# Performance work log

Hardware: AMD Instinct MI355X
Metric: run time of the kernel (lower is better)

## Reference

```python
import jax, jax.numpy as jnp
import numpy as np

B, IN_DIM, HID, OUT = 4096, 2048, 2048, 2048
BN_EPS = 1e-5


def setup_inputs() -> dict:
    key = jax.random.key(0)
    ks = jax.random.split(key, 4)
    s1 = 1.0 / np.sqrt(IN_DIM)
    s2 = 1.0 / np.sqrt(HID)
    return {
        "x1": jax.random.normal(ks[0], (B, IN_DIM), jnp.float32),
        "x2": jax.random.normal(ks[1], (B, IN_DIM), jnp.float32),
        "W1": jax.random.normal(ks[2], (IN_DIM, HID), jnp.float32) * s1,
        "b1": jnp.zeros((HID,), jnp.float32),
        "gamma": jnp.ones((HID,), jnp.float32),
        "beta": jnp.zeros((HID,), jnp.float32),
        "W2": jax.random.normal(ks[3], (HID, OUT), jnp.float32) * s2,
        "b2": jnp.zeros((OUT,), jnp.float32),
        "batch_size": B,
        "T": jnp.float32(0.2),
    }


def _predictor(x, W1, b1, gamma, beta, W2, b2):
    # Linear -> BatchNorm1d (training-mode batch stats, biased var) -> ReLU -> Linear
    h = x @ W1 + b1
    mu = jnp.mean(h, axis=0)
    var = jnp.var(h, axis=0)  # biased, matches torch BN normalization
    h = (h - mu) * jax.lax.rsqrt(var + BN_EPS) * gamma + beta
    h = jax.nn.relu(h)
    return h @ W2 + b2


def _off_diag(S):
    # S: [B, B] -> [B, B-1], row i keeps columns j != i (order preserved)
    n = S.shape[0]
    j = jnp.arange(n - 1)
    cols = j[None, :] + (j[None, :] >= jnp.arange(n)[:, None])
    return jnp.take_along_axis(S, cols, axis=1)


def _l2norm(x):
    return x / jnp.linalg.norm(x, axis=1, keepdims=True)


def reference(x1, x2, W1, b1, gamma, beta, W2, b2, batch_size, T):
    q1 = _l2norm(_predictor(x1, W1, b1, gamma, beta, W2, b2))
    q2 = _l2norm(_predictor(x2, W1, b1, gamma, beta, W2, b2))
    k1, k2 = q1, q2  # k = normalized q in the original

    l_pos1 = jnp.sum(q1 * k2, axis=1)  # [B]
    l_pos2 = jnp.sum(q2 * k1, axis=1)

    # per-row negatives: cat(q without self, k_other without self)
    neg1 = jnp.concatenate([_off_diag(q1 @ q1.T), _off_diag(q1 @ k2.T)], axis=1)
    neg2 = jnp.concatenate([_off_diag(q2 @ q2.T), _off_diag(q2 @ k1.T)], axis=1)

    logits1 = jnp.concatenate([l_pos1[:, None], neg1], axis=1) / T  # [B, 2B-1]
    logits2 = jnp.concatenate([l_pos2[:, None], neg2], axis=1) / T
    labels = jnp.zeros((q1.shape[0],), jnp.int32)
    return logits1, logits2, labels
```

## Files before the change

### kernel.cpp

```cpp
#include <hip/hip_runtime.h>
#include <stdint.h>

#define BATCH 4096
#define DIM   2048
#define LROW  8191

typedef __attribute__((ext_vector_type(8))) short bf16x8;
typedef __attribute__((ext_vector_type(4))) float f32x4;

typedef __attribute__((address_space(1))) void gvoid;
typedef __attribute__((address_space(3))) void lvoid;
#define GLOAD16(g, l) __builtin_amdgcn_global_load_lds((gvoid*)(g), (lvoid*)(l), 16, 0, 0)

__device__ __forceinline__ unsigned short f2bf(float f) {
    unsigned int u = __float_as_uint(f);
    return (unsigned short)((u + 0x7FFFu + ((u >> 16) & 1u)) >> 16);
}
__device__ __forceinline__ float bf2f(unsigned short s) {
    return __uint_as_float(((unsigned int)s) << 16);
}


__global__ __launch_bounds__(256) void k_cvt8(const float* __restrict__ src,
                                              unsigned short* __restrict__ dst) {
    size_t i = ((size_t)blockIdx.x * 256 + threadIdx.x) * 8;
    float4 v0 = *(const float4*)(src + i);
    float4 v1 = *(const float4*)(src + i + 4);
    bf16x8 p;
    p[0] = (short)f2bf(v0.x); p[1] = (short)f2bf(v0.y);
    p[2] = (short)f2bf(v0.z); p[3] = (short)f2bf(v0.w);
    p[4] = (short)f2bf(v1.x); p[5] = (short)f2bf(v1.y);
    p[6] = (short)f2bf(v1.z); p[7] = (short)f2bf(v1.w);
    *(bf16x8*)(dst + i) = p;
}

__global__ __launch_bounds__(256) void k_transpose_cvt(const float* __restrict__ W,
                                                       unsigned short* __restrict__ WT) {
    __shared__ unsigned short t[32][33];
    int n0 = blockIdx.x * 32, k0 = blockIdx.y * 32;
    int tx = threadIdx.x, ty = threadIdx.y;
#pragma unroll
    for (int i = 0; i < 4; i++) {
        int k = ty + i * 8;
        t[k][tx] = f2bf(W[(size_t)(k0 + k) * DIM + n0 + tx]);
    }
    __syncthreads();
#pragma unroll
    for (int i = 0; i < 4; i++) {
        int r = ty + i * 8;
        WT[(size_t)(n0 + r) * DIM + k0 + tx] = t[tx][r];
    }
}

template <int EPI>
__global__ __launch_bounds__(256) void k_gemm(const short* __restrict__ A_,
                                              const short* __restrict__ B_,
                                              void* __restrict__ out0,
                                              void* __restrict__ out1,
                                              const float* __restrict__ bias,
                                              float* __restrict__ st0,
                                              float* __restrict__ st1,
                                              const float* __restrict__ Tptr,
                                              int K) {
    __shared__ __align__(16) short smem[2 * 128 * 32];
    short* As = smem;
    short* Bs = smem + 128 * 32;

    const int tid = threadIdx.x;
    const int w = tid >> 6, l = tid & 63;
    const int wRow = (w >> 1) * 64, wCol = (w & 1) * 64;
    const int lr = l & 15, quad = l >> 4;

    int m0, n0, bi = 0, bj = 0;
    const short* A;
    const short* Bm;
    if (EPI == 2) {
        int t = blockIdx.x;
        while (t >= 32 - bi) { t -= 32 - bi; bi++; }
        bj = bi + t;
        m0 = bi * 128; n0 = bj * 128;
        const short* Q = A_ + (size_t)blockIdx.y * BATCH * DIM;
        A = Q; Bm = Q;
    } else {
        m0 = blockIdx.y * 128; n0 = blockIdx.x * 128;
        A = A_; Bm = B_;
    }

    const int c0 = w * 2, c1 = w * 2 + 1;
    const int lrow = l >> 2, lkoff = (l & 3) * 8;
    const short* gA0 = A + (size_t)(m0 + c0 * 16 + lrow) * K + lkoff;
    const short* gA1 = A + (size_t)(m0 + c1 * 16 + lrow) * K + lkoff;
    const short* gB0 = Bm + (size_t)(n0 + c0 * 16 + lrow) * K + lkoff;
    const short* gB1 = Bm + (size_t)(n0 + c1 * 16 + lrow) * K + lkoff;
    short* lA0 = As + c0 * 512; short* lA1 = As + c1 * 512;
    short* lB0 = Bs + c0 * 512; short* lB1 = Bs + c1 * 512;

    const int aoff = (wRow + lr) * 32 + quad * 8;
    const int boff = (wCol + lr) * 32 + quad * 8;

    f32x4 acc[4][4] = {};

    for (int k0 = 0; k0 < K; k0 += 32) {
        GLOAD16(gA0, lA0); GLOAD16(gA1, lA1);
        GLOAD16(gB0, lB0); GLOAD16(gB1, lB1);
        gA0 += 32; gA1 += 32; gB0 += 32; gB1 += 32;
        __syncthreads();

        bf16x8 af[4], bfr[4];
#pragma unroll
        for (int i = 0; i < 4; i++) {
            af[i]  = *(const bf16x8*)(As + aoff + i * 512);
            bfr[i] = *(const bf16x8*)(Bs + boff + i * 512);
        }
#pragma unroll
        for (int mi = 0; mi < 4; mi++)
#pragma unroll
            for (int ni = 0; ni < 4; ni++)
                acc[mi][ni] = __builtin_amdgcn_mfma_f32_16x16x32_bf16(af[mi], bfr[ni],
                                                                      acc[mi][ni], 0, 0, 0);
        __syncthreads();
    }

    if (EPI == 0) {
        unsigned short* H = (unsigned short*)out0;
        const int half = m0 >> 12;
        float s[4] = {0.f, 0.f, 0.f, 0.f}, s2[4] = {0.f, 0.f, 0.f, 0.f};
#pragma unroll
        for (int ni = 0; ni < 4; ni++) {
            int col = n0 + wCol + ni * 16 + lr;
            float bv = bias[col];
#pragma unroll
            for (int mi = 0; mi < 4; mi++) {
                int row = m0 + wRow + mi * 16 + quad * 4;
#pragma unroll
                for (int r = 0; r < 4; r++) {
                    float v = acc[mi][ni][r] + bv;
                    H[(size_t)(row + r) * DIM + col] = f2bf(v);
                    s[ni] += v; s2[ni] += v * v;
                }
            }
        }
#pragma unroll
        for (int ni = 0; ni < 4; ni++) {
            float a = s[ni], b = s2[ni];
            a += __shfl_xor(a, 16); b += __shfl_xor(b, 16);
            a += __shfl_xor(a, 32); b += __shfl_xor(b, 32);
            if (quad == 0) {
                int col = n0 + wCol + ni * 16 + lr;
                atomicAdd(&st0[half * DIM + col], a);
                atomicAdd(&st1[half * DIM + col], b);
            }
        }
    } else if (EPI == 1) {
        unsigned short* G = (unsigned short*)out0;
        float bv[4];
#pragma unroll
        for (int ni = 0; ni < 4; ni++) bv[ni] = bias[n0 + wCol + ni * 16 + lr];
#pragma unroll
        for (int mi = 0; mi < 4; mi++) {
            int rowb = m0 + wRow + mi * 16 + quad * 4;
#pragma unroll
            for (int r = 0; r < 4; r++) {
                int row = rowb + r;
                float p = 0.f;
#pragma unroll
                for (int ni = 0; ni < 4; ni++) {
                    int col = n0 + wCol + ni * 16 + lr;
                    float v = acc[mi][ni][r] + bv[ni];
                    G[(size_t)row * DIM + col] = f2bf(v);
                    p += v * v;
                }
                p += __shfl_xor(p, 1); p += __shfl_xor(p, 2);
                p += __shfl_xor(p, 4); p += __shfl_xor(p, 8);
                if (lr == 0) atomicAdd(&st0[row], p);
            }
        }
    } else {
        const float invT = 1.0f / Tptr[0];
        float* L  = (EPI == 2) ? (float*)(blockIdx.y ? out1 : out0) : (float*)out0;
        float* Lm = (EPI == 2) ? L : (float*)out1;
        const bool diagblk = (EPI == 2) && (bi == bj);
#pragma unroll
        for (int mi = 0; mi < 4; mi++) {
            int ibase = m0 + wRow + mi * 16 + quad * 4;
#pragma unroll
            for (int ni = 0; ni < 4; ni++) {
                int j = n0 + wCol + ni * 16 + lr;
#pragma unroll
                for (int r = 0; r < 4; r++) {
                    int i = ibase + r;
                    float v = acc[mi][ni][r] * invT;
                    int dc;
                    if (EPI == 2) {
                        if (diagblk) {
                            if (j == i) continue;
                            dc = 1 + j - (j > i);
                        } else {
                            dc = j;
                        }
                    } else {
                        dc = (j == i) ? 0 : (4096 + j - (j > i));
                    }
                    L[(size_t)i * LROW + dc] = v;
                }
            }
        }
        if (EPI == 3 || bi != bj) {
            float* tsc = (float*)smem + w * 320;
#pragma unroll
            for (int mi = 0; mi < 4; mi++) {
                int I0 = m0 + wRow + mi * 16;
#pragma unroll
                for (int ni = 0; ni < 4; ni++) {
                    int J0 = n0 + wCol + ni * 16;
#pragma unroll
                    for (int r = 0; r < 4; r++)
                        tsc[(quad * 4 + r) * 20 + lr] = acc[mi][ni][r];
                    int a = I0 + lr;
#pragma unroll
                    for (int r = 0; r < 4; r++) {
                        int b = J0 + quad * 4 + r;
                        float tv = tsc[lr * 20 + quad * 4 + r] * invT;
                        int dcm;
                        if (EPI == 2) dcm = 1 + a;
                        else dcm = (a == b) ? 0 : (4096 + a - (a > b));
                        Lm[(size_t)b * LROW + dcm] = tv;
                    }
                }
            }
        }
    }
}


__global__ __launch_bounds__(256) void k_bn_coef(float* __restrict__ musum,
                                                 float* __restrict__ sqsum,
                                                 const float* __restrict__ gamma,
                                                 const float* __restrict__ beta) {
    int i = blockIdx.x * 256 + threadIdx.x;
    int col = i & (DIM - 1);
    const float inv_n = 1.0f / 4096.0f;
    float mu = musum[i] * inv_n;
    float var = sqsum[i] * inv_n - mu * mu;
    float sc = rsqrtf(var + 1e-5f) * gamma[col];
    musum[i] = sc;
    sqsum[i] = beta[col] - mu * sc;
}

__global__ __launch_bounds__(256) void k_bn_apply(unsigned short* __restrict__ H,
                                                  const float* __restrict__ scale,
                                                  const float* __restrict__ shift) {
    size_t idx = ((size_t)blockIdx.x * 256 + threadIdx.x) * 8;
    int col = (int)(idx & (DIM - 1));
    int base = ((int)(idx >> 23)) * DIM + col;
    bf16x8 hv = *(bf16x8*)(H + idx);
    bf16x8 o;
#pragma unroll
    for (int t = 0; t < 8; t++) {
        float x = bf2f((unsigned short)hv[t]);
        x = fmaxf(x * scale[base + t] + shift[base + t], 0.f);
        o[t] = (short)f2bf(x);
    }
    *(bf16x8*)(H + idx) = o;
}

__global__ __launch_bounds__(256) void k_rowinv(float* __restrict__ rss) {
    int i = blockIdx.x * 256 + threadIdx.x;
    rss[i] = rsqrtf(rss[i]);
}

__global__ __launch_bounds__(256) void k_qnorm(const unsigned short* __restrict__ G,
                                               const float* __restrict__ inv,
                                               unsigned short* __restrict__ Q) {
    size_t idx = ((size_t)blockIdx.x * 256 + threadIdx.x) * 8;
    float iv = inv[idx >> 11];
    bf16x8 g = *(const bf16x8*)(G + idx);
    bf16x8 o;
#pragma unroll
    for (int t = 0; t < 8; t++) o[t] = (short)f2bf(bf2f((unsigned short)g[t]) * iv);
    *(bf16x8*)(Q + idx) = o;
}


extern "C" void kernel_launch(void* const* d_in, const int* in_sizes, int n_in,
                              void* d_out, int out_size, void* d_ws, size_t ws_size,
                              hipStream_t stream) {
    const float* x1    = (const float*)d_in[0];
    const float* x2    = (const float*)d_in[1];
    const float* W1    = (const float*)d_in[2];
    const float* b1    = (const float*)d_in[3];
    const float* gamma = (const float*)d_in[4];
    const float* beta  = (const float*)d_in[5];
    const float* W2    = (const float*)d_in[6];
    const float* b2    = (const float*)d_in[7];
    const float* Tp    = (const float*)d_in[9];
    float* out = (float*)d_out;

    char* ws = (char*)d_ws;
    unsigned short* R1  = (unsigned short*)ws;
    unsigned short* R3  = (unsigned short*)(ws + (32ull << 20));
    unsigned short* W1T = (unsigned short*)(ws + (64ull << 20));
    unsigned short* W2T = (unsigned short*)(ws + (72ull << 20));
    float* musum = (float*)(ws + (80ull << 20));
    float* sqsum = musum + 2 * DIM;
    float* rss   = sqsum + 2 * DIM;

    hipMemsetAsync(musum, 0, (4 * DIM + 8192) * sizeof(float), stream);

    k_cvt8<<<4096, 256, 0, stream>>>(x1, R1);
    k_cvt8<<<4096, 256, 0, stream>>>(x2, R1 + (size_t)BATCH * DIM);
    k_transpose_cvt<<<dim3(64, 64), dim3(32, 8), 0, stream>>>(W1, W1T);
    k_transpose_cvt<<<dim3(64, 64), dim3(32, 8), 0, stream>>>(W2, W2T);

    k_gemm<0><<<dim3(16, 64), 256, 0, stream>>>((const short*)R1, (const short*)W1T,
                                                R3, nullptr, b1, musum, sqsum, nullptr, DIM);
    k_bn_coef<<<16, 256, 0, stream>>>(musum, sqsum, gamma, beta);
    k_bn_apply<<<8192, 256, 0, stream>>>(R3, musum, sqsum);

    k_gemm<1><<<dim3(16, 64), 256, 0, stream>>>((const short*)R3, (const short*)W2T,
                                                R1, nullptr, b2, rss, nullptr, nullptr, DIM);
    k_rowinv<<<32, 256, 0, stream>>>(rss);
    k_qnorm<<<8192, 256, 0, stream>>>(R1, rss, R3);

    const short* Q  = (const short*)R3;
    const short* Q2 = (const short*)(R3 + (size_t)BATCH * DIM);
    float* L1 = out;
    float* L2 = out + (size_t)BATCH * LROW;
    k_gemm<2><<<dim3(528, 2), 256, 0, stream>>>(Q, nullptr, L1, L2,
                                                nullptr, nullptr, nullptr, Tp, DIM);
    k_gemm<3><<<dim3(32, 32), 256, 0, stream>>>(Q, Q2, L1, L2,
                                                nullptr, nullptr, nullptr, Tp, DIM);

    hipMemsetAsync(out + (size_t)2 * BATCH * LROW, 0, BATCH * sizeof(int), stream);
}
```

Measured before the change: 831.6 us.

## Use 256x256 tiled pipelined GEMM, fold L2 normalization into logits epilogue

Replaces the 128x128 GEMM with a 512-thread 256x256 tile kernel that uses a multi-stage LDS ring of global-to-LDS loads, XOR-swizzled LDS addressing, and MFMA priority hints. The separate q-normalization pass is removed: the similarity GEMM now runs on unnormalized rows and scales each output by the inverse row norms in the epilogue. All four similarity blocks (q1q1, q1q2, q2q1, q2q2) become one symmetric upper-triangular launch over the stacked 8192 rows, with mirrored writes. This aims for more data reuse per tile and fewer kernel launches and passes, at the cost of 128 KB of LDS, higher register pressure, and a slightly different rounding order.

```diff
diff --git a/kernel.cpp b/kernel.cpp
--- a/kernel.cpp
+++ b/kernel.cpp
@@ -53,87 +53,140 @@
 }
 
 template <int EPI>
-__global__ __launch_bounds__(256) void k_gemm(const short* __restrict__ A_,
-                                              const short* __restrict__ B_,
-                                              void* __restrict__ out0,
-                                              void* __restrict__ out1,
-                                              const float* __restrict__ bias,
-                                              float* __restrict__ st0,
-                                              float* __restrict__ st1,
-                                              const float* __restrict__ Tptr,
-                                              int K) {
-    __shared__ __align__(16) short smem[2 * 128 * 32];
-    short* As = smem;
-    short* Bs = smem + 128 * 32;
-
-    const int tid = threadIdx.x;
-    const int w = tid >> 6, l = tid & 63;
-    const int wRow = (w >> 1) * 64, wCol = (w & 1) * 64;
-    const int lr = l & 15, quad = l >> 4;
+__global__ __launch_bounds__(512, 2) void k_g256(const short* __restrict__ A_,
+                                                 const short* __restrict__ B_,
+                                                 void* __restrict__ out0,
+                                                 void* __restrict__ out1,
+                                                 const float* __restrict__ bias,
+                                                 float* __restrict__ st0,
+                                                 float* __restrict__ st1,
+                                                 const float* __restrict__ Tptr,
+                                                 int K) {
+    __shared__ __align__(16) char smem[131072];
+
+    const int tid  = threadIdx.x;
+    const int w    = tid >> 6;
+    const int l    = tid & 63;
+    const int lr   = l & 15;
+    const int quad = l >> 4;
+    const int wm   = w >> 2;
+    const int wn   = w & 3;
 
     int m0, n0, bi = 0, bj = 0;
-    const short* A;
-    const short* Bm;
     if (EPI == 2) {
         int t = blockIdx.x;
         while (t >= 32 - bi) { t -= 32 - bi; bi++; }
         bj = bi + t;
-        m0 = bi * 128; n0 = bj * 128;
-        const short* Q = A_ + (size_t)blockIdx.y * BATCH * DIM;
-        A = Q; Bm = Q;
+        m0 = bi * 256; n0 = bj * 256;
     } else {
-        m0 = blockIdx.y * 128; n0 = blockIdx.x * 128;
-        A = A_; Bm = B_;
-    }
-
-    const int c0 = w * 2, c1 = w * 2 + 1;
-    const int lrow = l >> 2, lkoff = (l & 3) * 8;
-    const short* gA0 = A + (size_t)(m0 + c0 * 16 + lrow) * K + lkoff;
-    const short* gA1 = A + (size_t)(m0 + c1 * 16 + lrow) * K + lkoff;
-    const short* gB0 = Bm + (size_t)(n0 + c0 * 16 + lrow) * K + lkoff;
-    const short* gB1 = Bm + (size_t)(n0 + c1 * 16 + lrow) * K + lkoff;
-    short* lA0 = As + c0 * 512; short* lA1 = As + c1 * 512;
-    short* lB0 = Bs + c0 * 512; short* lB1 = Bs + c1 * 512;
-
-    const int aoff = (wRow + lr) * 32 + quad * 8;
-    const int boff = (wCol + lr) * 32 + quad * 8;
-
-    f32x4 acc[4][4] = {};
-
-    for (int k0 = 0; k0 < K; k0 += 32) {
-        GLOAD16(gA0, lA0); GLOAD16(gA1, lA1);
-        GLOAD16(gB0, lB0); GLOAD16(gB1, lB1);
-        gA0 += 32; gA1 += 32; gB0 += 32; gB1 += 32;
-        __syncthreads();
-
-        bf16x8 af[4], bfr[4];
-#pragma unroll
-        for (int i = 0; i < 4; i++) {
-            af[i]  = *(const bf16x8*)(As + aoff + i * 512);
-            bfr[i] = *(const bf16x8*)(Bs + boff + i * 512);
-        }
-#pragma unroll
-        for (int mi = 0; mi < 4; mi++)
-#pragma unroll
-            for (int ni = 0; ni < 4; ni++)
-                acc[mi][ni] = __builtin_amdgcn_mfma_f32_16x16x32_bf16(af[mi], bfr[ni],
-                                                                      acc[mi][ni], 0, 0, 0);
-        __syncthreads();
-    }
+        m0 = blockIdx.y * 256; n0 = blockIdx.x * 256;
+    }
+
+    const int NT = K >> 6;
+    const size_t rsb = (size_t)K * 2;
+
+    const unsigned soff = (unsigned)((w * 1024 + l * 16) ^ (l & 32));
+    const int rowS = soff >> 6;
+    const int kbS  = soff & 63;
+    const char* APan = (const char*)A_ + (size_t)(m0 + rowS) * rsb + kbS;
+    const char* BPan = (const char*)B_ + (size_t)(n0 + rowS) * rsb + kbS;
+    const size_t row128 = rsb << 7;
+    char* ldsS = smem + w * 1024;
+
+    const int laneoff = (lr * 64 + quad * 16) ^ ((lr & 8) << 2);
+    const char* ldsA = smem + wm * 8192 + laneoff;
+    const char* ldsB = smem + wn * 4096 + laneoff;
+
+    f32x4 acc[8][4] = {};
+    bf16x8 aq[4], bq[4];
+
+    auto STAGE = [&](int ht) {
+        if (ht < 4 * NT) {
+            const size_t koff = (size_t)((ht >> 2) * 128 + ((ht >> 1) & 1) * 64);
+            char* d = ldsS + ((ht & 7) << 14);
+            const char* s = (ht & 1) ? (APan + koff) : (BPan + koff);
+            GLOAD16(s, d);
+            GLOAD16(s + row128, d + 8192);
+        }
+    };
+
+#define MM16(mh)                                                                     \
+    _Pragma("unroll") for (int mi = 0; mi < 4; ++mi) {                               \
+        _Pragma("unroll") for (int ni = 0; ni < 4; ++ni) {                           \
+            acc[(mh) * 4 + mi][ni] = __builtin_amdgcn_mfma_f32_16x16x32_bf16(        \
+                aq[mi], bq[ni], acc[(mh) * 4 + mi][ni], 0, 0, 0);                    \
+        }                                                                            \
+    }
+#define BAR()   __builtin_amdgcn_s_barrier()
+#define LGKM0() asm volatile("s_waitcnt lgkmcnt(0)" ::: "memory")
+
+    for (int ht = 0; ht < 7; ++ht) STAGE(ht);
+    asm volatile("s_waitcnt vmcnt(6)" ::: "memory");
+    BAR();
+
+    int htn = 7;
+    for (int t = 0; t < NT; ++t) {
+        const int s0 = (t & 1) << 2;
+#pragma unroll
+        for (int ni = 0; ni < 4; ++ni)
+            bq[ni] = *(const bf16x8*)(ldsB + (s0 << 14) + ni * 1024);
+#pragma unroll
+        for (int mi = 0; mi < 4; ++mi)
+            aq[mi] = *(const bf16x8*)(ldsA + ((s0 + 1) << 14) + mi * 1024);
+        STAGE(htn); ++htn;
+        BAR(); LGKM0();
+        __builtin_amdgcn_s_setprio(1);
+        MM16(0)
+        __builtin_amdgcn_s_setprio(0);
+        BAR();
+#pragma unroll
+        for (int mi = 0; mi < 4; ++mi)
+            aq[mi] = *(const bf16x8*)(ldsA + ((s0 + 1) << 14) + 4096 + mi * 1024);
+        STAGE(htn); ++htn;
+        BAR(); LGKM0();
+        __builtin_amdgcn_s_setprio(1);
+        MM16(1)
+        __builtin_amdgcn_s_setprio(0);
+        BAR();
+#pragma unroll
+        for (int ni = 0; ni < 4; ++ni)
+            bq[ni] = *(const bf16x8*)(ldsB + ((s0 + 2) << 14) + ni * 1024);
+#pragma unroll
+        for (int mi = 0; mi < 4; ++mi)
+            aq[mi] = *(const bf16x8*)(ldsA + ((s0 + 3) << 14) + mi * 1024);
+        STAGE(htn); ++htn;
+        BAR(); LGKM0();
+        __builtin_amdgcn_s_setprio(1);
+        MM16(0)
+        __builtin_amdgcn_s_setprio(0);
+        BAR();
+#pragma unroll
+        for (int mi = 0; mi < 4; ++mi)
+            aq[mi] = *(const bf16x8*)(ldsA + ((s0 + 3) << 14) + 4096 + mi * 1024);
+        STAGE(htn); ++htn;
+        BAR(); LGKM0();
+        __builtin_amdgcn_s_setprio(1);
+        MM16(1)
+        __builtin_amdgcn_s_setprio(0);
+        if (t < NT - 2) { asm volatile("s_waitcnt vmcnt(6)" ::: "memory"); }
+        else            { asm volatile("s_waitcnt vmcnt(0)" ::: "memory"); }
+        BAR();
+    }
+#undef MM16
 
     if (EPI == 0) {
         unsigned short* H = (unsigned short*)out0;
         const int half = m0 >> 12;
-        float s[4] = {0.f, 0.f, 0.f, 0.f}, s2[4] = {0.f, 0.f, 0.f, 0.f};
-#pragma unroll
-        for (int ni = 0; ni < 4; ni++) {
-            int col = n0 + wCol + ni * 16 + lr;
-            float bv = bias[col];
-#pragma unroll
-            for (int mi = 0; mi < 4; mi++) {
-                int row = m0 + wRow + mi * 16 + quad * 4;
-#pragma unroll
-                for (int r = 0; r < 4; r++) {
+        float s[4] = {}, s2[4] = {};
+#pragma unroll
+        for (int ni = 0; ni < 4; ++ni) {
+            const int col = n0 + wn * 64 + ni * 16 + lr;
+            const float bv = bias[col];
+#pragma unroll
+            for (int mi = 0; mi < 8; ++mi) {
+                const int row = m0 + wm * 128 + mi * 16 + quad * 4;
+#pragma unroll
+                for (int r = 0; r < 4; ++r) {
                     float v = acc[mi][ni][r] + bv;
                     H[(size_t)(row + r) * DIM + col] = f2bf(v);
                     s[ni] += v; s2[ni] += v * v;
@@ -141,12 +194,12 @@
             }
         }
 #pragma unroll
-        for (int ni = 0; ni < 4; ni++) {
+        for (int ni = 0; ni < 4; ++ni) {
             float a = s[ni], b = s2[ni];
             a += __shfl_xor(a, 16); b += __shfl_xor(b, 16);
             a += __shfl_xor(a, 32); b += __shfl_xor(b, 32);
             if (quad == 0) {
-                int col = n0 + wCol + ni * 16 + lr;
+                const int col = n0 + wn * 64 + ni * 16 + lr;
                 atomicAdd(&st0[half * DIM + col], a);
                 atomicAdd(&st1[half * DIM + col], b);
             }
@@ -155,17 +208,17 @@
         unsigned short* G = (unsigned short*)out0;
         float bv[4];
 #pragma unroll
-        for (int ni = 0; ni < 4; ni++) bv[ni] = bias[n0 + wCol + ni * 16 + lr];
-#pragma unroll
-        for (int mi = 0; mi < 4; mi++) {
-            int rowb = m0 + wRow + mi * 16 + quad * 4;
-#pragma unroll
-            for (int r = 0; r < 4; r++) {
-                int row = rowb + r;
+        for (int ni = 0; ni < 4; ++ni) bv[ni] = bias[n0 + wn * 64 + ni * 16 + lr];
+#pragma unroll
+        for (int mi = 0; mi < 8; ++mi) {
+            const int rowb = m0 + wm * 128 + mi * 16 + quad * 4;
+#pragma unroll
+            for (int r = 0; r < 4; ++r) {
+                const int row = rowb + r;
                 float p = 0.f;
 #pragma unroll
-                for (int ni = 0; ni < 4; ni++) {
-                    int col = n0 + wCol + ni * 16 + lr;
+                for (int ni = 0; ni < 4; ++ni) {
+                    const int col = n0 + wn * 64 + ni * 16 + lr;
                     float v = acc[mi][ni][r] + bv[ni];
                     G[(size_t)row * DIM + col] = f2bf(v);
                     p += v * v;
@@ -177,59 +230,72 @@
         }
     } else {
         const float invT = 1.0f / Tptr[0];
-        float* L  = (EPI == 2) ? (float*)(blockIdx.y ? out1 : out0) : (float*)out0;
-        float* Lm = (EPI == 2) ? L : (float*)out1;
-        const bool diagblk = (EPI == 2) && (bi == bj);
-#pragma unroll
-        for (int mi = 0; mi < 4; mi++) {
-            int ibase = m0 + wRow + mi * 16 + quad * 4;
-#pragma unroll
-            for (int ni = 0; ni < 4; ni++) {
-                int j = n0 + wCol + ni * 16 + lr;
-#pragma unroll
-                for (int r = 0; r < 4; r++) {
-                    int i = ibase + r;
-                    float v = acc[mi][ni][r] * invT;
+        const float* inv = st0;
+        float* L1v = (float*)out0;
+        float* L2v = (float*)out1;
+        const bool crossm = (bi < 16) && (bj >= 16);
+        const bool diagb  = (bi == bj);
+        float* Lw = (bi < 16) ? L1v : L2v;
+        float* Lm = (bj < 16) ? L1v : L2v;
+        const int rbase = (bi < 16) ? 0 : 4096;
+        const int cbase = (bj < 16) ? 0 : 4096;
+
+        float ri[8][4], cj[4];
+#pragma unroll
+        for (int mi = 0; mi < 8; ++mi)
+#pragma unroll
+            for (int r = 0; r < 4; ++r)
+                ri[mi][r] = inv[m0 + wm * 128 + mi * 16 + quad * 4 + r] * invT;
+#pragma unroll
+        for (int ni = 0; ni < 4; ++ni) cj[ni] = inv[n0 + wn * 64 + ni * 16 + lr];
+
+#pragma unroll
+        for (int mi = 0; mi < 8; ++mi) {
+            const int ib = m0 + wm * 128 + mi * 16 + quad * 4 - rbase;
+#pragma unroll
+            for (int ni = 0; ni < 4; ++ni) {
+                const int jl = n0 + wn * 64 + ni * 16 + lr - cbase;
+#pragma unroll
+                for (int r = 0; r < 4; ++r) {
+                    const int il = ib + r;
+                    const float v = acc[mi][ni][r] * ri[mi][r] * cj[ni];
                     int dc;
-                    if (EPI == 2) {
-                        if (diagblk) {
-                            if (j == i) continue;
-                            dc = 1 + j - (j > i);
-                        } else {
-                            dc = j;
-                        }
+                    if (crossm) {
+                        dc = (jl == il) ? 0 : (4096 + jl - (jl > il));
                     } else {
-                        dc = (j == i) ? 0 : (4096 + j - (j > i));
+                        if (jl == il) continue;
+                        dc = 1 + jl - (jl > il);
                     }
-                    L[(size_t)i * LROW + dc] = v;
+                    Lw[(size_t)il * LROW + dc] = v;
                 }
             }
         }
-        if (EPI == 3 || bi != bj) {
+        if (!diagb) {
             float* tsc = (float*)smem + w * 320;
 #pragma unroll
-            for (int mi = 0; mi < 4; mi++) {
-                int I0 = m0 + wRow + mi * 16;
-#pragma unroll
-                for (int ni = 0; ni < 4; ni++) {
-                    int J0 = n0 + wCol + ni * 16;
-#pragma unroll
-                    for (int r = 0; r < 4; r++)
-                        tsc[(quad * 4 + r) * 20 + lr] = acc[mi][ni][r];
-                    int a = I0 + lr;
-#pragma unroll
-                    for (int r = 0; r < 4; r++) {
-                        int b = J0 + quad * 4 + r;
-                        float tv = tsc[lr * 20 + quad * 4 + r] * invT;
+            for (int mi = 0; mi < 8; ++mi) {
+                const int al = m0 + wm * 128 + mi * 16 + lr - rbase;
+#pragma unroll
+                for (int ni = 0; ni < 4; ++ni) {
+                    const int J0 = n0 + wn * 64 + ni * 16 - cbase;
+#pragma unroll
+                    for (int r = 0; r < 4; ++r)
+                        tsc[(quad * 4 + r) * 20 + lr] = acc[mi][ni][r] * ri[mi][r] * cj[ni];
+#pragma unroll
+                    for (int r = 0; r < 4; ++r) {
+                        const int bl = J0 + quad * 4 + r;
+                        const float tv = tsc[lr * 20 + quad * 4 + r];
                         int dcm;
-                        if (EPI == 2) dcm = 1 + a;
-                        else dcm = (a == b) ? 0 : (4096 + a - (a > b));
-                        Lm[(size_t)b * LROW + dcm] = tv;
+                        if (crossm) dcm = (al == bl) ? 0 : (4096 + al - (al > bl));
+                        else        dcm = 1 + al - (al > bl);
+                        Lm[(size_t)bl * LROW + dcm] = tv;
                     }
                 }
             }
         }
     }
+#undef BAR
+#undef LGKM0
 }
 
 
@@ -267,18 +333,6 @@
 __global__ __launch_bounds__(256) void k_rowinv(float* __restrict__ rss) {
     int i = blockIdx.x * 256 + threadIdx.x;
     rss[i] = rsqrtf(rss[i]);
-}
-
-__global__ __launch_bounds__(256) void k_qnorm(const unsigned short* __restrict__ G,
-                                               const float* __restrict__ inv,
-                                               unsigned short* __restrict__ Q) {
-    size_t idx = ((size_t)blockIdx.x * 256 + threadIdx.x) * 8;
-    float iv = inv[idx >> 11];
-    bf16x8 g = *(const bf16x8*)(G + idx);
-    bf16x8 o;
-#pragma unroll
-    for (int t = 0; t < 8; t++) o[t] = (short)f2bf(bf2f((unsigned short)g[t]) * iv);
-    *(bf16x8*)(Q + idx) = o;
 }
 
 
@@ -312,24 +366,19 @@
     k_transpose_cvt<<<dim3(64, 64), dim3(32, 8), 0, stream>>>(W1, W1T);
     k_transpose_cvt<<<dim3(64, 64), dim3(32, 8), 0, stream>>>(W2, W2T);
 
-    k_gemm<0><<<dim3(16, 64), 256, 0, stream>>>((const short*)R1, (const short*)W1T,
-                                                R3, nullptr, b1, musum, sqsum, nullptr, DIM);
+    k_g256<0><<<dim3(8, 32), 512, 0, stream>>>((const short*)R1, (const short*)W1T,
+                                               R3, nullptr, b1, musum, sqsum, nullptr, DIM);
     k_bn_coef<<<16, 256, 0, stream>>>(musum, sqsum, gamma, beta);
     k_bn_apply<<<8192, 256, 0, stream>>>(R3, musum, sqsum);
 
-    k_gemm<1><<<dim3(16, 64), 256, 0, stream>>>((const short*)R3, (const short*)W2T,
-                                                R1, nullptr, b2, rss, nullptr, nullptr, DIM);
+    k_g256<1><<<dim3(8, 32), 512, 0, stream>>>((const short*)R3, (const short*)W2T,
+                                               R1, nullptr, b2, rss, nullptr, nullptr, DIM);
     k_rowinv<<<32, 256, 0, stream>>>(rss);
-    k_qnorm<<<8192, 256, 0, stream>>>(R1, rss, R3);
-
-    const short* Q  = (const short*)R3;
-    const short* Q2 = (const short*)(R3 + (size_t)BATCH * DIM);
+
     float* L1 = out;
     float* L2 = out + (size_t)BATCH * LROW;
-    k_gemm<2><<<dim3(528, 2), 256, 0, stream>>>(Q, nullptr, L1, L2,
-                                                nullptr, nullptr, nullptr, Tp, DIM);
-    k_gemm<3><<<dim3(32, 32), 256, 0, stream>>>(Q, Q2, L1, L2,
-                                                nullptr, nullptr, nullptr, Tp, DIM);
+    k_g256<2><<<dim3(528, 1), 512, 0, stream>>>((const short*)R1, (const short*)R1,
+                                                L1, L2, nullptr, rss, nullptr, Tp, DIM);
 
     hipMemsetAsync(out + (size_t)2 * BATCH * LROW, 0, BATCH * sizeof(int), stream);
 }
```

Result: faster. 731.5 us (-12.0%).
